# Optimization experiments

Hardware: AMD Instinct MI355X
Metric: run time of the kernel (lower is better)

Reference implementation:

```python
import jax, jax.numpy as jnp
import numpy as np

N_NODES = 50000
N_EDGES = 800000
IN_FEATS = 64
HID_FEATS = 64


def setup_inputs() -> dict:
    key = jax.random.key(0)
    ks = jax.random.split(key, 5)
    x = jax.random.normal(ks[0], (N_NODES, IN_FEATS), dtype=jnp.float32)
    src = jax.random.randint(ks[1], (N_EDGES,), 0, N_NODES)
    dst = jax.random.randint(ks[2], (N_EDGES,), 0, N_NODES)
    # GraphConv parameters (Glorot-ish init, bias zeros as in dgl defaults)
    W1 = jax.random.normal(ks[3], (IN_FEATS, HID_FEATS), dtype=jnp.float32) / np.sqrt(IN_FEATS)
    b1 = jnp.zeros((HID_FEATS,), dtype=jnp.float32)
    W2 = jax.random.normal(ks[4], (HID_FEATS, IN_FEATS), dtype=jnp.float32) / np.sqrt(HID_FEATS)
    b2 = jnp.zeros((IN_FEATS,), dtype=jnp.float32)
    return {"x": x, "src": src, "dst": dst, "W1": W1, "b1": b1, "W2": W2, "b2": b2}


def _graph_conv(x, src, dst, W, b, n_nodes):
    """dgl GraphConv with norm='both': D_dst^{-1/2} A D_src^{-1/2} X W + b."""
    ones = jnp.ones((src.shape[0],), dtype=x.dtype)
    deg_out = jax.ops.segment_sum(ones, src, num_segments=n_nodes)
    deg_in = jax.ops.segment_sum(ones, dst, num_segments=n_nodes)
    norm_out = jnp.where(deg_out > 0, jax.lax.rsqrt(jnp.maximum(deg_out, 1.0)), 0.0)
    norm_in = jnp.where(deg_in > 0, jax.lax.rsqrt(jnp.maximum(deg_in, 1.0)), 0.0)
    h = x * norm_out[:, None]                                  # [N, F] scaled by src norm
    agg = jax.ops.segment_sum(h[src], dst, num_segments=n_nodes)  # gather over edges + scatter-add
    return (agg * norm_in[:, None]) @ W + b


def reference(x, src, dst, W1, b1, W2, b2):
    n, d = x.shape
    # dHdx: conv -> tanh -> conv
    y = jnp.tanh(_graph_conv(x, src, dst, W1, b1, n))
    y = _graph_conv(y, src, dst, W2, b2, n)
    # J = cat([I[d//2:], -I[:d//2]])  -> symplectic [[0, I], [-I, 0]]
    I = jnp.eye(d, dtype=x.dtype)
    J = jnp.concatenate([I[d // 2:], -I[: d // 2]], axis=0)
    # get_D is undefined in the source module; treated as zero dissipation term.
    return y @ J.T
```

## Files before the change

### kernel.cpp

```cpp
#include <hip/hip_runtime.h>
#include <hip/hip_bf16.h>
#include <math.h>

#define N_NODES 50000
#define N_EDGES 800000
#define F 64
#define NPAD 50048
#define NBLK ((N_NODES + 255) / 256)

#define P_HIST 256
#define CHUNK (N_EDGES / P_HIST)
#define WORDS8 12500
#define RBLK8 ((WORDS8 + 255) / 256)

#define TW 20
#define RV3BLK (WORDS8 / TW)
#define TS 260

#define LROW 36
#define LBLK ((N_NODES + 31) / 32)

typedef short short8 __attribute__((ext_vector_type(8)));
typedef float f32x4 __attribute__((ext_vector_type(4)));

__device__ inline unsigned short f2bf(float f) {
    unsigned u = __float_as_uint(f);
    unsigned r = (u + 0x7fffu + ((u >> 16) & 1u)) >> 16;
    return (unsigned short)r;
}
__device__ inline float bf2f(unsigned v) { return __uint_as_float(v << 16); }
__device__ inline float bf2f_hi(unsigned v) { return __uint_as_float(v & 0xffff0000u); }

__device__ inline unsigned wave_incl_scan(unsigned v, int lane) {
    #pragma unroll
    for (int d = 1; d < 64; d <<= 1) {
        unsigned u = __shfl_up(v, d, 64);
        if (lane >= d) v += u;
    }
    return v;
}


__global__ __launch_bounds__(256) void hist_kernel(
    const int* __restrict__ src, const int* __restrict__ dst,
    unsigned* __restrict__ histd, unsigned* __restrict__ deg_out_u)
{
    __shared__ unsigned lds[WORDS8];
    int p = blockIdx.x, t = threadIdx.x;
    int e0 = p * CHUNK;
    for (int i = t; i < WORDS8; i += 256) lds[i] = 0;
    for (int i = t; i < CHUNK; i += 256)
        atomicAdd(&deg_out_u[src[e0 + i]], 1u);
    __syncthreads();
    for (int i = t; i < CHUNK; i += 256) {
        int v = dst[e0 + i];
        atomicAdd(&lds[v >> 2], 1u << ((v & 3) * 8));
    }
    __syncthreads();
    unsigned* outp = histd + (size_t)p * WORDS8;
    for (int i = t; i < WORDS8; i += 256) outp[i] = lds[i];
}

__global__ __launch_bounds__(256) void reduce_v3_kernel(
    unsigned* __restrict__ histd,
    float* __restrict__ norm_in,
    int* __restrict__ row_off, unsigned* __restrict__ wordsum)
{
    __shared__ unsigned lds[TW * TS];
    int t = threadIdx.x, b = blockIdx.x;
    int lane = t & 63, ww = t >> 6;
    int w0 = b * TW;

    {
        uint4* gp = (uint4*)(histd + (size_t)t * WORDS8 + w0);
        #pragma unroll
        for (int i = 0; i < TW / 4; ++i) {
            uint4 v = gp[i];
            lds[(i * 4 + 0) * TS + t] = v.x;
            lds[(i * 4 + 1) * TS + t] = v.y;
            lds[(i * 4 + 2) * TS + t] = v.z;
            lds[(i * 4 + 3) * TS + t] = v.w;
        }
    }
    __syncthreads();
    #pragma unroll
    for (int k = 0; k < TW / 4; ++k) {
        int lw = ww + k * 4;
        uint4 h = *(uint4*)(lds + lw * TS + 4 * lane);
        unsigned lsum = h.x + h.y + h.z + h.w;
        unsigned inc = lsum;
        #pragma unroll
        for (int d = 1; d < 64; d <<= 1) {
            unsigned u = __shfl_up(inc, d, 64);
            if (lane >= d) inc += u;
        }
        unsigned run = inc - lsum;
        uint4 o;
        o.x = run; run += h.x;
        o.y = run; run += h.y;
        o.z = run; run += h.z;
        o.w = run;
        *(uint4*)(lds + lw * TS + 4 * lane) = o;
        unsigned total = __shfl(inc, 63, 64);
        if (lane == 0) {
            int w = w0 + lw;
            unsigned d0 = total & 255u, d1 = (total >> 8) & 255u;
            unsigned d2 = (total >> 16) & 255u, d3 = total >> 24;
            norm_in[4 * w]     = d0 ? rsqrtf((float)d0) : 0.f;
            norm_in[4 * w + 1] = d1 ? rsqrtf((float)d1) : 0.f;
            norm_in[4 * w + 2] = d2 ? rsqrtf((float)d2) : 0.f;
            norm_in[4 * w + 3] = d3 ? rsqrtf((float)d3) : 0.f;
            int4 r;
            r.x = 0; r.y = (int)d0; r.z = (int)(d0 + d1); r.w = (int)(d0 + d1 + d2);
            *(int4*)(row_off + 4 * w) = r;
            wordsum[w] = d0 + d1 + d2 + d3;
        }
    }
    __syncthreads();
    {
        uint4* gp = (uint4*)(histd + (size_t)t * WORDS8 + w0);
        #pragma unroll
        for (int i = 0; i < TW / 4; ++i) {
            uint4 v;
            v.x = lds[(i * 4 + 0) * TS + t];
            v.y = lds[(i * 4 + 1) * TS + t];
            v.z = lds[(i * 4 + 2) * TS + t];
            v.w = lds[(i * 4 + 3) * TS + t];
            gp[i] = v;
        }
    }
}

__global__ __launch_bounds__(256) void scanw_kernel(
    const unsigned* __restrict__ wordsum, int* __restrict__ row_off,
    unsigned* __restrict__ blockSums,
    const unsigned* __restrict__ deg_out_u, float* __restrict__ norm_out)
{
    __shared__ unsigned wsum[4];
    int t = threadIdx.x, b = blockIdx.x;
    int w = b * 256 + t;
    unsigned v = (w < WORDS8) ? wordsum[w] : 0u;
    int lane = t & 63, wid = t >> 6;
    unsigned inc = wave_incl_scan(v, lane);
    if (lane == 63) wsum[wid] = inc;
    __syncthreads();
    if (t == 0) {
        unsigned acc = 0;
        #pragma unroll
        for (int q = 0; q < 4; ++q) { unsigned x = wsum[q]; wsum[q] = acc; acc += x; }
    }
    __syncthreads();
    unsigned excl = inc - v + wsum[wid];
    if (w < WORDS8) {
        int4 r = *(int4*)(row_off + 4 * w);
        r.x += (int)excl; r.y += (int)excl; r.z += (int)excl; r.w += (int)excl;
        *(int4*)(row_off + 4 * w) = r;
        uint4 dg = *(const uint4*)(deg_out_u + 4 * w);
        float4 nv;
        nv.x = dg.x ? rsqrtf((float)dg.x) : 0.f;
        nv.y = dg.y ? rsqrtf((float)dg.y) : 0.f;
        nv.z = dg.z ? rsqrtf((float)dg.z) : 0.f;
        nv.w = dg.w ? rsqrtf((float)dg.w) : 0.f;
        *(float4*)(norm_out + 4 * w) = nv;
    }
    if (t == 255) blockSums[b] = excl + v;
}

__global__ __launch_bounds__(256) void scan_fin_kernel(
    const unsigned* __restrict__ blockSums, int* __restrict__ row_off)
{
    __shared__ unsigned off_s;
    int t = threadIdx.x, b = blockIdx.x;
    if (t < 64) {
        unsigned v = (t < b) ? blockSums[t] : 0u;
        #pragma unroll
        for (int d = 1; d < 64; d <<= 1) v += __shfl_xor(v, d, 64);
        if (t == 0) off_s = v;
    }
    __syncthreads();
    int off = (int)off_s;
    int w = b * 256 + t;
    if (w < WORDS8) {
        int4 r = *(int4*)(row_off + 4 * w);
        r.x += off; r.y += off; r.z += off; r.w += off;
        *(int4*)(row_off + 4 * w) = r;
    }
    if (w == 0) row_off[N_NODES] = N_EDGES;
}

__global__ __launch_bounds__(256) void scatter_kernel(
    const int* __restrict__ src, const int* __restrict__ dst,
    const int* __restrict__ row_off, const unsigned* __restrict__ histd,
    int* __restrict__ csr_src)
{
    __shared__ unsigned lds[WORDS8];
    int p = blockIdx.x, t = threadIdx.x;
    int e0 = p * CHUNK;
    const unsigned* pref = histd + (size_t)p * WORDS8;
    for (int i = t; i < WORDS8; i += 256) lds[i] = 0;
    __syncthreads();
    for (int i = t; i < CHUNK; i += 256) {
        int d = dst[e0 + i];
        int sh = (d & 3) * 8;
        unsigned old = atomicAdd(&lds[d >> 2], 1u << sh);
        unsigned rank = (old >> sh) & 255u;
        unsigned pre  = (pref[d >> 2] >> sh) & 255u;
        csr_src[row_off[d] + (int)(pre + rank)] = src[e0 + i];
    }
}


__global__ __launch_bounds__(256) void degrees_kernel(
    const int* __restrict__ src, const int* __restrict__ dst,
    unsigned* __restrict__ deg_out_u, unsigned* __restrict__ deg_in_u)
{
    int e = blockIdx.x * 256 + threadIdx.x;
    if (e < N_EDGES) {
        atomicAdd(&deg_out_u[src[e]], 1u);
        atomicAdd(&deg_in_u[dst[e]], 1u);
    }
}

__global__ __launch_bounds__(256) void fb_scan_a_kernel(
    const unsigned* __restrict__ deg_in_u, const unsigned* __restrict__ deg_out_u,
    float* __restrict__ norm_out, float* __restrict__ norm_in,
    int* __restrict__ row_off, unsigned* __restrict__ blockSums)
{
    __shared__ unsigned wsum[4];
    int t = threadIdx.x, b = blockIdx.x;
    int idx = b * 256 + t;
    unsigned v = 0, dout = 0;
    if (idx < N_NODES) { v = deg_in_u[idx]; dout = deg_out_u[idx]; }
    int lane = t & 63, wid = t >> 6;
    unsigned inc = wave_incl_scan(v, lane);
    if (lane == 63) wsum[wid] = inc;
    __syncthreads();
    if (t == 0) {
        unsigned acc = 0;
        #pragma unroll
        for (int q = 0; q < 4; ++q) { unsigned x = wsum[q]; wsum[q] = acc; acc += x; }
    }
    __syncthreads();
    unsigned excl = inc - v + wsum[wid];
    if (idx < N_NODES) {
        row_off[idx] = (int)excl;
        norm_in[idx]  = v    ? rsqrtf((float)v)    : 0.f;
        norm_out[idx] = dout ? rsqrtf((float)dout) : 0.f;
    }
    if (t == 255) blockSums[b] = excl + v;
}

__global__ __launch_bounds__(256) void fb_scan_b_kernel(
    const unsigned* __restrict__ blockSums, unsigned* __restrict__ blockOff, int cnt)
{
    __shared__ unsigned wsum[4];
    int t = threadIdx.x;
    unsigned v = (t < cnt) ? blockSums[t] : 0u;
    int lane = t & 63, wid = t >> 6;
    unsigned inc = wave_incl_scan(v, lane);
    if (lane == 63) wsum[wid] = inc;
    __syncthreads();
    if (t == 0) {
        unsigned acc = 0;
        #pragma unroll
        for (int q = 0; q < 4; ++q) { unsigned x = wsum[q]; wsum[q] = acc; acc += x; }
    }
    __syncthreads();
    if (t < cnt) blockOff[t] = inc - v + wsum[wid];
}

__global__ __launch_bounds__(256) void fb_scan_c_kernel(
    const unsigned* __restrict__ blockOff, int* __restrict__ row_off,
    unsigned* __restrict__ cursor)
{
    int idx = blockIdx.x * 256 + threadIdx.x;
    if (idx < N_NODES) {
        int v = row_off[idx] + (int)blockOff[blockIdx.x];
        row_off[idx] = v;
        cursor[idx] = (unsigned)v;
    }
    if (idx == 0) row_off[N_NODES] = N_EDGES;
}

__global__ __launch_bounds__(256) void fb_csr_fill_kernel(
    const int* __restrict__ src, const int* __restrict__ dst,
    unsigned* __restrict__ cursor, int* __restrict__ csr_src)
{
    int e = blockIdx.x * 256 + threadIdx.x;
    if (e < N_EDGES) {
        unsigned p = atomicAdd(&cursor[dst[e]], 1u);
        csr_src[p] = src[e];
    }
}


__global__ __launch_bounds__(256) void prescale_kernel(
    const float* __restrict__ x, const float* __restrict__ norm_out,
    unsigned* __restrict__ xb)
{
    int t = blockIdx.x * 256 + threadIdx.x;
    if (t < N_NODES * 32) {
        int n = t >> 5;
        float w = norm_out[n];
        float2 v = ((const float2*)x)[t];
        xb[t] = (unsigned)f2bf(v.x * w) | ((unsigned)f2bf(v.y * w) << 16);
    }
}

__device__ inline void block_agg32(
    const unsigned* __restrict__ tab, const float* __restrict__ norm_in,
    const int* __restrict__ row_off, const int* __restrict__ csr_src,
    int nb, unsigned* lds)
{
    int tid = threadIdx.x;
    int wid = tid >> 6, lane = tid & 63;
    int g = lane >> 3, lp = lane & 7;
    int m = wid * 8 + g;
    int n = nb + m;
    float a0 = 0.f, a1 = 0.f, a2 = 0.f, a3 = 0.f;
    float a4 = 0.f, a5 = 0.f, a6 = 0.f, a7 = 0.f;
    float w = 0.f;
    if (n < N_NODES) {
        int beg = row_off[n];
        int end = row_off[n + 1];
        w = norm_in[n];
        int e = beg;
        for (; e + 3 < end; e += 4) {
            int s0 = csr_src[e], s1 = csr_src[e + 1];
            int s2 = csr_src[e + 2], s3 = csr_src[e + 3];
            uint4 v0 = *(const uint4*)(tab + (size_t)s0 * 32 + lp * 4);
            uint4 v1 = *(const uint4*)(tab + (size_t)s1 * 32 + lp * 4);
            uint4 v2 = *(const uint4*)(tab + (size_t)s2 * 32 + lp * 4);
            uint4 v3 = *(const uint4*)(tab + (size_t)s3 * 32 + lp * 4);
            a0 += bf2f(v0.x & 0xffffu); a1 += bf2f_hi(v0.x);
            a2 += bf2f(v0.y & 0xffffu); a3 += bf2f_hi(v0.y);
            a4 += bf2f(v0.z & 0xffffu); a5 += bf2f_hi(v0.z);
            a6 += bf2f(v0.w & 0xffffu); a7 += bf2f_hi(v0.w);
            a0 += bf2f(v1.x & 0xffffu); a1 += bf2f_hi(v1.x);
            a2 += bf2f(v1.y & 0xffffu); a3 += bf2f_hi(v1.y);
            a4 += bf2f(v1.z & 0xffffu); a5 += bf2f_hi(v1.z);
            a6 += bf2f(v1.w & 0xffffu); a7 += bf2f_hi(v1.w);
            a0 += bf2f(v2.x & 0xffffu); a1 += bf2f_hi(v2.x);
            a2 += bf2f(v2.y & 0xffffu); a3 += bf2f_hi(v2.y);
            a4 += bf2f(v2.z & 0xffffu); a5 += bf2f_hi(v2.z);
            a6 += bf2f(v2.w & 0xffffu); a7 += bf2f_hi(v2.w);
            a0 += bf2f(v3.x & 0xffffu); a1 += bf2f_hi(v3.x);
            a2 += bf2f(v3.y & 0xffffu); a3 += bf2f_hi(v3.y);
            a4 += bf2f(v3.z & 0xffffu); a5 += bf2f_hi(v3.z);
            a6 += bf2f(v3.w & 0xffffu); a7 += bf2f_hi(v3.w);
        }
        for (; e < end; ++e) {
            int s0 = csr_src[e];
            uint4 v0 = *(const uint4*)(tab + (size_t)s0 * 32 + lp * 4);
            a0 += bf2f(v0.x & 0xffffu); a1 += bf2f_hi(v0.x);
            a2 += bf2f(v0.y & 0xffffu); a3 += bf2f_hi(v0.y);
            a4 += bf2f(v0.z & 0xffffu); a5 += bf2f_hi(v0.z);
            a6 += bf2f(v0.w & 0xffffu); a7 += bf2f_hi(v0.w);
        }
    }
    uint4 o;
    o.x = (unsigned)f2bf(a0 * w) | ((unsigned)f2bf(a1 * w) << 16);
    o.y = (unsigned)f2bf(a2 * w) | ((unsigned)f2bf(a3 * w) << 16);
    o.z = (unsigned)f2bf(a4 * w) | ((unsigned)f2bf(a5 * w) << 16);
    o.w = (unsigned)f2bf(a6 * w) | ((unsigned)f2bf(a7 * w) << 16);
    *(uint4*)(lds + m * LROW + lp * 4) = o;
}

__global__ __launch_bounds__(256) void layer1_fused_kernel(
    const unsigned* __restrict__ tab, const float* __restrict__ norm_in,
    const float* __restrict__ norm_out, const int* __restrict__ row_off,
    const int* __restrict__ csr_src, const float* __restrict__ Wm,
    const float* __restrict__ bias, unsigned short* __restrict__ hb)
{
    __shared__ unsigned lds[32 * LROW];
    int tid = threadIdx.x;
    int wid = tid >> 6, lane = tid & 63;
    int q = lane >> 4, lp16 = lane & 15;
    int nb = blockIdx.x * 32;

    short8 bfrag[2];
    #pragma unroll
    for (int kt = 0; kt < 2; ++kt)
        #pragma unroll
        for (int j = 0; j < 8; ++j)
            bfrag[kt][j] = (short)f2bf(Wm[(kt * 32 + q * 8 + j) * F + wid * 16 + lp16]);

    block_agg32(tab, norm_in, row_off, csr_src, nb, lds);
    __syncthreads();

    int nn = wid * 16 + lp16;
    float bv = bias[nn];
    #pragma unroll
    for (int rg = 0; rg < 2; ++rg) {
        short8 afrag[2];
        #pragma unroll
        for (int kt = 0; kt < 2; ++kt)
            afrag[kt] = *(const short8*)(lds + (rg * 16 + lp16) * LROW + kt * 16 + q * 4);
        f32x4 acc = (f32x4){0.f, 0.f, 0.f, 0.f};
        #pragma unroll
        for (int kt = 0; kt < 2; ++kt)
            acc = __builtin_amdgcn_mfma_f32_16x16x32_bf16(afrag[kt], bfrag[kt], acc, 0, 0, 0);
        #pragma unroll
        for (int r = 0; r < 4; ++r) {
            int row = nb + rg * 16 + q * 4 + r;
            if (row < N_NODES) {
                float z = tanhf(acc[r] + bv) * norm_out[row];
                hb[(size_t)row * F + nn] = f2bf(z);
            }
        }
    }
}

__global__ __launch_bounds__(256) void layer2_fused_kernel(
    const unsigned* __restrict__ tab, const float* __restrict__ norm_in,
    const int* __restrict__ row_off, const int* __restrict__ csr_src,
    const float* __restrict__ Wm, const float* __restrict__ bias,
    float* __restrict__ out)
{
    __shared__ unsigned lds[32 * LROW];
    int tid = threadIdx.x;
    int wid = tid >> 6, lane = tid & 63;
    int q = lane >> 4, lp16 = lane & 15;
    int nb = blockIdx.x * 32;

    short8 bfrag[2];
    #pragma unroll
    for (int kt = 0; kt < 2; ++kt)
        #pragma unroll
        for (int j = 0; j < 8; ++j)
            bfrag[kt][j] = (short)f2bf(Wm[(kt * 32 + q * 8 + j) * F + wid * 16 + lp16]);

    block_agg32(tab, norm_in, row_off, csr_src, nb, lds);
    __syncthreads();

    int nn = wid * 16 + lp16;
    float bv = bias[nn];
    int oc = (nn + 32) & 63;
    float sgn = (nn < 32) ? -1.f : 1.f;
    #pragma unroll
    for (int rg = 0; rg < 2; ++rg) {
        short8 afrag[2];
        #pragma unroll
        for (int kt = 0; kt < 2; ++kt)
            afrag[kt] = *(const short8*)(lds + (rg * 16 + lp16) * LROW + kt * 16 + q * 4);
        f32x4 acc = (f32x4){0.f, 0.f, 0.f, 0.f};
        #pragma unroll
        for (int kt = 0; kt < 2; ++kt)
            acc = __builtin_amdgcn_mfma_f32_16x16x32_bf16(afrag[kt], bfrag[kt], acc, 0, 0, 0);
        #pragma unroll
        for (int r = 0; r < 4; ++r) {
            int row = nb + rg * 16 + q * 4 + r;
            if (row < N_NODES) {
                float z = acc[r] + bv;
                out[(size_t)row * F + oc] = sgn * z;
            }
        }
    }
}

extern "C" void kernel_launch(void* const* d_in, const int* in_sizes, int n_in,
                              void* d_out, int out_size, void* d_ws, size_t ws_size,
                              hipStream_t stream) {
    const float* x   = (const float*)d_in[0];
    const int*   src = (const int*)d_in[1];
    const int*   dst = (const int*)d_in[2];
    const float* W1  = (const float*)d_in[3];
    const float* b1  = (const float*)d_in[4];
    const float* W2  = (const float*)d_in[5];
    const float* b2  = (const float*)d_in[6];
    float* out = (float*)d_out;

    unsigned* ws = (unsigned*)d_ws;
    float*    norm_out = (float*)ws;
    float*    norm_in  = (float*)(ws + NPAD);
    int*      row_off  = (int*)(ws + 2 * NPAD);
    int*      csr_src  = (int*)(ws + 3 * NPAD);
    unsigned* xb       = ws + 3 * NPAD + N_EDGES;
    unsigned* hbu      = xb + (size_t)NPAD * 32;
    unsigned* blockSums= hbu + (size_t)NPAD * 32;
    unsigned* blockOff = blockSums + 256;
    unsigned* wordsum  = blockOff + 256;
    unsigned* deg_out_u= wordsum + WORDS8;
    unsigned* tail     = deg_out_u + NPAD;
    unsigned* histd = tail;
    size_t need_new = ((size_t)(tail - ws) + (size_t)P_HIST * WORDS8) * 4;

    if (ws_size >= need_new) {
        hipMemsetAsync(deg_out_u, 0, NPAD * sizeof(unsigned), stream);
        hist_kernel<<<P_HIST, 256, 0, stream>>>(src, dst, histd, deg_out_u);
        reduce_v3_kernel<<<RV3BLK, 256, 0, stream>>>(histd, norm_in, row_off, wordsum);
        scanw_kernel<<<RBLK8, 256, 0, stream>>>(wordsum, row_off, blockSums, deg_out_u, norm_out);
        scan_fin_kernel<<<RBLK8, 256, 0, stream>>>(blockSums, row_off);
        scatter_kernel<<<P_HIST, 256, 0, stream>>>(src, dst, row_off, histd, csr_src);
    } else {
        unsigned* deg_out_f = tail;
        unsigned* deg_in_f  = tail + NPAD;
        unsigned* cursor_f  = tail + 2 * NPAD;
        hipMemsetAsync(deg_out_f, 0, 2 * NPAD * sizeof(unsigned), stream);
        degrees_kernel<<<(N_EDGES + 255) / 256, 256, 0, stream>>>(src, dst, deg_out_f, deg_in_f);
        fb_scan_a_kernel<<<NBLK, 256, 0, stream>>>(deg_in_f, deg_out_f, norm_out, norm_in, row_off, blockSums);
        fb_scan_b_kernel<<<1, 256, 0, stream>>>(blockSums, blockOff, NBLK);
        fb_scan_c_kernel<<<NBLK, 256, 0, stream>>>(blockOff, row_off, cursor_f);
        fb_csr_fill_kernel<<<(N_EDGES + 255) / 256, 256, 0, stream>>>(src, dst, cursor_f, csr_src);
    }

    prescale_kernel<<<(N_NODES * 32 + 255) / 256, 256, 0, stream>>>(x, norm_out, xb);
    layer1_fused_kernel<<<LBLK, 256, 0, stream>>>(
        xb, norm_in, norm_out, row_off, csr_src, W1, b1, (unsigned short*)hbu);

    layer2_fused_kernel<<<LBLK, 256, 0, stream>>>(
        hbu, norm_in, row_off, csr_src, W2, b2, out);
}
```

Measured before the change: 200.7 us.

## Replace histogram-based CSR build with global atomic degree count and cursor fill

Removes the per-block LDS histogram path (hist, transposed reduce, two scan passes, deterministic scatter) and always uses the simpler path: global atomic degree counts, block scan, then atomic-cursor CSR fill. The separate block-offset scan and apply kernels are merged into one kernel where each block reduces its own prefix of block sums. This cuts kernel launches and the large 256x12500 histogram buffer traffic. In exchange, edge order within each row becomes nondeterministic and the fill relies on contended global atomics.

```diff
diff --git a/kernel.cpp b/kernel.cpp
--- a/kernel.cpp
+++ b/kernel.cpp
@@ -7,15 +7,8 @@
 #define F 64
 #define NPAD 50048
 #define NBLK ((N_NODES + 255) / 256)
-
-#define P_HIST 256
-#define CHUNK (N_EDGES / P_HIST)
-#define WORDS8 12500
-#define RBLK8 ((WORDS8 + 255) / 256)
-
-#define TW 20
-#define RV3BLK (WORDS8 / TW)
-#define TS 260
+#define EBLK ((N_EDGES + 255) / 256)
+
 
 #define LROW 36
 #define LBLK ((N_NODES + 31) / 32)
@@ -41,175 +34,6 @@
 }
 
 
-__global__ __launch_bounds__(256) void hist_kernel(
-    const int* __restrict__ src, const int* __restrict__ dst,
-    unsigned* __restrict__ histd, unsigned* __restrict__ deg_out_u)
-{
-    __shared__ unsigned lds[WORDS8];
-    int p = blockIdx.x, t = threadIdx.x;
-    int e0 = p * CHUNK;
-    for (int i = t; i < WORDS8; i += 256) lds[i] = 0;
-    for (int i = t; i < CHUNK; i += 256)
-        atomicAdd(&deg_out_u[src[e0 + i]], 1u);
-    __syncthreads();
-    for (int i = t; i < CHUNK; i += 256) {
-        int v = dst[e0 + i];
-        atomicAdd(&lds[v >> 2], 1u << ((v & 3) * 8));
-    }
-    __syncthreads();
-    unsigned* outp = histd + (size_t)p * WORDS8;
-    for (int i = t; i < WORDS8; i += 256) outp[i] = lds[i];
-}
-
-__global__ __launch_bounds__(256) void reduce_v3_kernel(
-    unsigned* __restrict__ histd,
-    float* __restrict__ norm_in,
-    int* __restrict__ row_off, unsigned* __restrict__ wordsum)
-{
-    __shared__ unsigned lds[TW * TS];
-    int t = threadIdx.x, b = blockIdx.x;
-    int lane = t & 63, ww = t >> 6;
-    int w0 = b * TW;
-
-    {
-        uint4* gp = (uint4*)(histd + (size_t)t * WORDS8 + w0);
-        #pragma unroll
-        for (int i = 0; i < TW / 4; ++i) {
-            uint4 v = gp[i];
-            lds[(i * 4 + 0) * TS + t] = v.x;
-            lds[(i * 4 + 1) * TS + t] = v.y;
-            lds[(i * 4 + 2) * TS + t] = v.z;
-            lds[(i * 4 + 3) * TS + t] = v.w;
-        }
-    }
-    __syncthreads();
-    #pragma unroll
-    for (int k = 0; k < TW / 4; ++k) {
-        int lw = ww + k * 4;
-        uint4 h = *(uint4*)(lds + lw * TS + 4 * lane);
-        unsigned lsum = h.x + h.y + h.z + h.w;
-        unsigned inc = lsum;
-        #pragma unroll
-        for (int d = 1; d < 64; d <<= 1) {
-            unsigned u = __shfl_up(inc, d, 64);
-            if (lane >= d) inc += u;
-        }
-        unsigned run = inc - lsum;
-        uint4 o;
-        o.x = run; run += h.x;
-        o.y = run; run += h.y;
-        o.z = run; run += h.z;
-        o.w = run;
-        *(uint4*)(lds + lw * TS + 4 * lane) = o;
-        unsigned total = __shfl(inc, 63, 64);
-        if (lane == 0) {
-            int w = w0 + lw;
-            unsigned d0 = total & 255u, d1 = (total >> 8) & 255u;
-            unsigned d2 = (total >> 16) & 255u, d3 = total >> 24;
-            norm_in[4 * w]     = d0 ? rsqrtf((float)d0) : 0.f;
-            norm_in[4 * w + 1] = d1 ? rsqrtf((float)d1) : 0.f;
-            norm_in[4 * w + 2] = d2 ? rsqrtf((float)d2) : 0.f;
-            norm_in[4 * w + 3] = d3 ? rsqrtf((float)d3) : 0.f;
-            int4 r;
-            r.x = 0; r.y = (int)d0; r.z = (int)(d0 + d1); r.w = (int)(d0 + d1 + d2);
-            *(int4*)(row_off + 4 * w) = r;
-            wordsum[w] = d0 + d1 + d2 + d3;
-        }
-    }
-    __syncthreads();
-    {
-        uint4* gp = (uint4*)(histd + (size_t)t * WORDS8 + w0);
-        #pragma unroll
-        for (int i = 0; i < TW / 4; ++i) {
-            uint4 v;
-            v.x = lds[(i * 4 + 0) * TS + t];
-            v.y = lds[(i * 4 + 1) * TS + t];
-            v.z = lds[(i * 4 + 2) * TS + t];
-            v.w = lds[(i * 4 + 3) * TS + t];
-            gp[i] = v;
-        }
-    }
-}
-
-__global__ __launch_bounds__(256) void scanw_kernel(
-    const unsigned* __restrict__ wordsum, int* __restrict__ row_off,
-    unsigned* __restrict__ blockSums,
-    const unsigned* __restrict__ deg_out_u, float* __restrict__ norm_out)
-{
-    __shared__ unsigned wsum[4];
-    int t = threadIdx.x, b = blockIdx.x;
-    int w = b * 256 + t;
-    unsigned v = (w < WORDS8) ? wordsum[w] : 0u;
-    int lane = t & 63, wid = t >> 6;
-    unsigned inc = wave_incl_scan(v, lane);
-    if (lane == 63) wsum[wid] = inc;
-    __syncthreads();
-    if (t == 0) {
-        unsigned acc = 0;
-        #pragma unroll
-        for (int q = 0; q < 4; ++q) { unsigned x = wsum[q]; wsum[q] = acc; acc += x; }
-    }
-    __syncthreads();
-    unsigned excl = inc - v + wsum[wid];
-    if (w < WORDS8) {
-        int4 r = *(int4*)(row_off + 4 * w);
-        r.x += (int)excl; r.y += (int)excl; r.z += (int)excl; r.w += (int)excl;
-        *(int4*)(row_off + 4 * w) = r;
-        uint4 dg = *(const uint4*)(deg_out_u + 4 * w);
-        float4 nv;
-        nv.x = dg.x ? rsqrtf((float)dg.x) : 0.f;
-        nv.y = dg.y ? rsqrtf((float)dg.y) : 0.f;
-        nv.z = dg.z ? rsqrtf((float)dg.z) : 0.f;
-        nv.w = dg.w ? rsqrtf((float)dg.w) : 0.f;
-        *(float4*)(norm_out + 4 * w) = nv;
-    }
-    if (t == 255) blockSums[b] = excl + v;
-}
-
-__global__ __launch_bounds__(256) void scan_fin_kernel(
-    const unsigned* __restrict__ blockSums, int* __restrict__ row_off)
-{
-    __shared__ unsigned off_s;
-    int t = threadIdx.x, b = blockIdx.x;
-    if (t < 64) {
-        unsigned v = (t < b) ? blockSums[t] : 0u;
-        #pragma unroll
-        for (int d = 1; d < 64; d <<= 1) v += __shfl_xor(v, d, 64);
-        if (t == 0) off_s = v;
-    }
-    __syncthreads();
-    int off = (int)off_s;
-    int w = b * 256 + t;
-    if (w < WORDS8) {
-        int4 r = *(int4*)(row_off + 4 * w);
-        r.x += off; r.y += off; r.z += off; r.w += off;
-        *(int4*)(row_off + 4 * w) = r;
-    }
-    if (w == 0) row_off[N_NODES] = N_EDGES;
-}
-
-__global__ __launch_bounds__(256) void scatter_kernel(
-    const int* __restrict__ src, const int* __restrict__ dst,
-    const int* __restrict__ row_off, const unsigned* __restrict__ histd,
-    int* __restrict__ csr_src)
-{
-    __shared__ unsigned lds[WORDS8];
-    int p = blockIdx.x, t = threadIdx.x;
-    int e0 = p * CHUNK;
-    const unsigned* pref = histd + (size_t)p * WORDS8;
-    for (int i = t; i < WORDS8; i += 256) lds[i] = 0;
-    __syncthreads();
-    for (int i = t; i < CHUNK; i += 256) {
-        int d = dst[e0 + i];
-        int sh = (d & 3) * 8;
-        unsigned old = atomicAdd(&lds[d >> 2], 1u << sh);
-        unsigned rank = (old >> sh) & 255u;
-        unsigned pre  = (pref[d >> 2] >> sh) & 255u;
-        csr_src[row_off[d] + (int)(pre + rank)] = src[e0 + i];
-    }
-}
-
-
 __global__ __launch_bounds__(256) void degrees_kernel(
     const int* __restrict__ src, const int* __restrict__ dst,
     unsigned* __restrict__ deg_out_u, unsigned* __restrict__ deg_in_u)
@@ -221,7 +45,7 @@
     }
 }
 
-__global__ __launch_bounds__(256) void fb_scan_a_kernel(
+__global__ __launch_bounds__(256) void scan_a_kernel(
     const unsigned* __restrict__ deg_in_u, const unsigned* __restrict__ deg_out_u,
     float* __restrict__ norm_out, float* __restrict__ norm_in,
     int* __restrict__ row_off, unsigned* __restrict__ blockSums)
@@ -250,39 +74,31 @@
     if (t == 255) blockSums[b] = excl + v;
 }
 
-__global__ __launch_bounds__(256) void fb_scan_b_kernel(
-    const unsigned* __restrict__ blockSums, unsigned* __restrict__ blockOff, int cnt)
+__global__ __launch_bounds__(256) void scan_bc_kernel(
+    const unsigned* __restrict__ blockSums, int* __restrict__ row_off,
+    unsigned* __restrict__ cursor)
 {
     __shared__ unsigned wsum[4];
-    int t = threadIdx.x;
-    unsigned v = (t < cnt) ? blockSums[t] : 0u;
+    __shared__ unsigned off_s;
+    int t = threadIdx.x, b = blockIdx.x;
+    unsigned v = (t < b) ? blockSums[t] : 0u;
     int lane = t & 63, wid = t >> 6;
-    unsigned inc = wave_incl_scan(v, lane);
-    if (lane == 63) wsum[wid] = inc;
-    __syncthreads();
-    if (t == 0) {
-        unsigned acc = 0;
-        #pragma unroll
-        for (int q = 0; q < 4; ++q) { unsigned x = wsum[q]; wsum[q] = acc; acc += x; }
-    }
-    __syncthreads();
-    if (t < cnt) blockOff[t] = inc - v + wsum[wid];
-}
-
-__global__ __launch_bounds__(256) void fb_scan_c_kernel(
-    const unsigned* __restrict__ blockOff, int* __restrict__ row_off,
-    unsigned* __restrict__ cursor)
-{
-    int idx = blockIdx.x * 256 + threadIdx.x;
+    #pragma unroll
+    for (int d = 1; d < 64; d <<= 1) v += __shfl_xor(v, d, 64);
+    if (lane == 0) wsum[wid] = v;
+    __syncthreads();
+    if (t == 0) off_s = wsum[0] + wsum[1] + wsum[2] + wsum[3];
+    __syncthreads();
+    int idx = b * 256 + t;
     if (idx < N_NODES) {
-        int v = row_off[idx] + (int)blockOff[blockIdx.x];
-        row_off[idx] = v;
-        cursor[idx] = (unsigned)v;
+        int r = row_off[idx] + (int)off_s;
+        row_off[idx] = r;
+        cursor[idx] = (unsigned)r;
     }
     if (idx == 0) row_off[N_NODES] = N_EDGES;
 }
 
-__global__ __launch_bounds__(256) void fb_csr_fill_kernel(
+__global__ __launch_bounds__(256) void csr_fill_kernel(
     const int* __restrict__ src, const int* __restrict__ dst,
     unsigned* __restrict__ cursor, int* __restrict__ csr_src)
 {
@@ -471,38 +287,22 @@
     float* out = (float*)d_out;
 
     unsigned* ws = (unsigned*)d_ws;
-    float*    norm_out = (float*)ws;
-    float*    norm_in  = (float*)(ws + NPAD);
-    int*      row_off  = (int*)(ws + 2 * NPAD);
-    int*      csr_src  = (int*)(ws + 3 * NPAD);
-    unsigned* xb       = ws + 3 * NPAD + N_EDGES;
-    unsigned* hbu      = xb + (size_t)NPAD * 32;
-    unsigned* blockSums= hbu + (size_t)NPAD * 32;
-    unsigned* blockOff = blockSums + 256;
-    unsigned* wordsum  = blockOff + 256;
-    unsigned* deg_out_u= wordsum + WORDS8;
-    unsigned* tail     = deg_out_u + NPAD;
-    unsigned* histd = tail;
-    size_t need_new = ((size_t)(tail - ws) + (size_t)P_HIST * WORDS8) * 4;
-
-    if (ws_size >= need_new) {
-        hipMemsetAsync(deg_out_u, 0, NPAD * sizeof(unsigned), stream);
-        hist_kernel<<<P_HIST, 256, 0, stream>>>(src, dst, histd, deg_out_u);
-        reduce_v3_kernel<<<RV3BLK, 256, 0, stream>>>(histd, norm_in, row_off, wordsum);
-        scanw_kernel<<<RBLK8, 256, 0, stream>>>(wordsum, row_off, blockSums, deg_out_u, norm_out);
-        scan_fin_kernel<<<RBLK8, 256, 0, stream>>>(blockSums, row_off);
-        scatter_kernel<<<P_HIST, 256, 0, stream>>>(src, dst, row_off, histd, csr_src);
-    } else {
-        unsigned* deg_out_f = tail;
-        unsigned* deg_in_f  = tail + NPAD;
-        unsigned* cursor_f  = tail + 2 * NPAD;
-        hipMemsetAsync(deg_out_f, 0, 2 * NPAD * sizeof(unsigned), stream);
-        degrees_kernel<<<(N_EDGES + 255) / 256, 256, 0, stream>>>(src, dst, deg_out_f, deg_in_f);
-        fb_scan_a_kernel<<<NBLK, 256, 0, stream>>>(deg_in_f, deg_out_f, norm_out, norm_in, row_off, blockSums);
-        fb_scan_b_kernel<<<1, 256, 0, stream>>>(blockSums, blockOff, NBLK);
-        fb_scan_c_kernel<<<NBLK, 256, 0, stream>>>(blockOff, row_off, cursor_f);
-        fb_csr_fill_kernel<<<(N_EDGES + 255) / 256, 256, 0, stream>>>(src, dst, cursor_f, csr_src);
-    }
+    float*    norm_out  = (float*)ws;
+    float*    norm_in   = (float*)(ws + NPAD);
+    int*      row_off   = (int*)(ws + 2 * NPAD);
+    int*      csr_src   = (int*)(ws + 3 * NPAD);
+    unsigned* xb        = ws + 3 * NPAD + N_EDGES;
+    unsigned* hbu       = xb + (size_t)NPAD * 32;
+    unsigned* blockSums = hbu + (size_t)NPAD * 32;
+    unsigned* deg_out_u = blockSums + 256;
+    unsigned* deg_in_u  = deg_out_u + NPAD;
+    unsigned* cursor    = deg_in_u + NPAD;
+
+    hipMemsetAsync(deg_out_u, 0, 2 * NPAD * sizeof(unsigned), stream);
+    degrees_kernel<<<EBLK, 256, 0, stream>>>(src, dst, deg_out_u, deg_in_u);
+    scan_a_kernel<<<NBLK, 256, 0, stream>>>(deg_in_u, deg_out_u, norm_out, norm_in, row_off, blockSums);
+    scan_bc_kernel<<<NBLK, 256, 0, stream>>>(blockSums, row_off, cursor);
+    csr_fill_kernel<<<EBLK, 256, 0, stream>>>(src, dst, cursor, csr_src);
 
     prescale_kernel<<<(N_NODES * 32 + 255) / 256, 256, 0, stream>>>(x, norm_out, xb);
     layer1_fused_kernel<<<LBLK, 256, 0, stream>>>(
```

Result: slower. 247.2 us (+23.2%).
